# Optimization experiments

Measured on AMD Instinct MI355X. Metric: run time of the kernel, lower is better.

The kernel has to match this reference:

```python
import jax, jax.numpy as jnp
import numpy as np

N, E, F, K = 20000, 320000, 64, 256


def _lin(k, fan_in, shape):
    s = 1.0 / np.sqrt(fan_in)
    return jax.random.uniform(k, shape, jnp.float32, -s, s)


def setup_inputs() -> dict:
    key = jax.random.key(0)
    ks = jax.random.split(key, 18)
    x = jax.random.normal(ks[0], (N, F), jnp.float32)
    row = jax.random.randint(ks[1], (E,), 0, N, jnp.int32)
    off = jax.random.randint(ks[2], (E,), 1, N, jnp.int32)
    col = (row + off) % N  # no self-loops; they are added inside reference
    edge_index = jnp.stack([row, col])
    return {
        "x": x,
        "edge_index": edge_index,
        # GCN conv stack (embedding_sizes=[64,64,64] -> two convs)
        "W0": _lin(ks[3], F, (F, F)), "b0": _lin(ks[4], F, (F,)),
        "W1": _lin(ks[5], F, (F, F)), "b1": _lin(ks[6], F, (F,)),
        # ASAPooling: lin(F,F), att(2F,1)
        "lin_W": _lin(ks[7], F, (F, F)), "lin_b": _lin(ks[8], F, (F,)),
        "att_W": _lin(ks[9], 2 * F, (2 * F,)), "att_b": _lin(ks[10], 2 * F, ()),
        # LEConv(F,1): lin1 (bias), lin2 (no bias), lin3 (bias)
        "le1_W": _lin(ks[11], F, (F,)), "le1_b": _lin(ks[12], F, ()),
        "le2_W": _lin(ks[13], F, (F,)),
        "le3_W": _lin(ks[14], F, (F,)), "le3_b": _lin(ks[15], F, ()),
    }


def reference(x, edge_index, W0, b0, W1, b1, lin_W, lin_b, att_W, att_b,
              le1_W, le1_b, le2_W, le3_W, le3_b):
    n = x.shape[0]
    loop = jnp.arange(n, dtype=edge_index.dtype)
    row = jnp.concatenate([edge_index[0], loop])  # source j
    col = jnp.concatenate([edge_index[1], loop])  # target i
    w = jnp.ones(row.shape[0], x.dtype)           # edge weights (incl. self-loops)

    # --- GCNConv stack (symmetric normalization, self-loops, weight 1) ---
    deg = jax.ops.segment_sum(w, col, num_segments=n)
    dis = jax.lax.rsqrt(deg)  # deg >= 1 thanks to self-loops
    norm = dis[row] * w * dis[col]

    def gcn(h, W, b):
        h = h @ W
        return jax.ops.segment_sum(norm[:, None] * h[row], col, num_segments=n) + b

    x = jax.nn.relu(gcn(x, W0, b0))
    x = jax.nn.relu(gcn(x, W1, b1))

    # --- ASAPooling attention scoring ---
    x_pool_j = x[row]                                            # [E', F]
    x_q = jax.ops.segment_max(x_pool_j, col, num_segments=n)    # max over incoming
    x_q = x_q @ lin_W + lin_b
    score = jnp.concatenate([x_q[col], x_pool_j], axis=-1) @ att_W + att_b  # [E']
    score = jax.nn.leaky_relu(score, 0.2)
    # segment softmax over target node
    smax = jax.ops.segment_max(score, col, num_segments=n)
    e = jnp.exp(score - smax[col])
    score = e / jax.ops.segment_sum(e, col, num_segments=n)[col]

    # cluster representations
    xc = jax.ops.segment_sum(x[row] * score[:, None], col, num_segments=n)  # [N, F]

    # --- LEConv fitness: sum_j w_ij*(lin1(x_j) - lin2(x_i)) + lin3(x_i) ---
    a = xc @ le1_W + le1_b
    b = xc @ le2_W
    agg = jax.ops.segment_sum(w * (a[row] - b[col]), col, num_segments=n)
    fitness = jax.nn.sigmoid(agg + xc @ le3_W + le3_b)           # [N]

    # --- top-k selection (single graph) ---
    fit_k, perm = jax.lax.top_k(fitness, K)
    x_new = xc[perm] * fit_k[:, None]                            # [K, F]

    # --- graph coarsening: A_new = S^T A S, S = score matrix cols at perm ---
    inv = jnp.full((n,), K, jnp.int32).at[perm].set(jnp.arange(K, dtype=jnp.int32))
    Sd = jnp.zeros((n, K + 1), x.dtype).at[row, inv[col]].add(score)
    S = Sd[:, :K]                                                # [N, K]
    AS = jax.ops.segment_sum(w[:, None] * S[col], row, num_segments=n)  # A @ S
    A_new = S.T @ AS                                             # [K, K]
    A_new = A_new.at[jnp.arange(K), jnp.arange(K)].set(1.0)      # fill_diag(1)

    return (x_new, A_new, perm)
```

## Files before the change

### kernel.cpp

```cpp
#include <hip/hip_runtime.h>
#include <math.h>

constexpr int N_ = 20000;
constexpr int E_ = 320000;
constexpr int M_ = E_ + N_;
constexpr int F_ = 64;
constexpr int K_ = 256;
constexpr int TCAP = 32768;
constexpr int OUT_WORDS = K_ * F_ + K_ * K_ + K_;

constexpr size_t O_RR   = 0;
constexpr size_t O_CC   = O_RR + M_;
constexpr size_t O_CSRC = O_CC + M_;
constexpr size_t O_CNRM = O_CSRC + M_;
constexpr size_t O_SC   = O_CNRM + M_;
constexpr size_t O_BUFA = O_SC + M_;
constexpr size_t O_BUFB = O_BUFA + (size_t)N_ * F_;
constexpr size_t O_BUFC = O_BUFB + (size_t)N_ * F_;
constexpr size_t O_CPTR = O_BUFC + (size_t)N_ * F_;
constexpr size_t O_Q2   = O_CPTR + N_ + 4;
constexpr size_t O_DEN  = O_Q2 + N_;
constexpr size_t O_AV   = O_DEN + N_;
constexpr size_t O_BV   = O_AV + N_;
constexpr size_t O_C3   = O_BV + N_;
constexpr size_t O_FIT  = O_C3 + N_;
constexpr size_t O_TPTR = O_FIT + N_;
constexpr size_t O_TI   = O_TPTR + N_ + 4;
constexpr size_t O_TK   = O_TI + TCAP;
constexpr size_t O_TV   = O_TK + TCAP;
constexpr size_t O_TIDX = O_TV + TCAP;
constexpr size_t O_PERM = O_TIDX + TCAP;
constexpr size_t O_FITS = O_PERM + K_;
constexpr size_t O_WQ   = O_FITS + K_;
constexpr size_t O_ZR   = O_WQ + 72;
constexpr size_t O_CNT  = O_ZR;
constexpr size_t O_CUR  = O_CNT + N_;
constexpr size_t O_TCNT = O_CUR + N_;
constexpr size_t O_TCUR = O_TCNT + N_;
constexpr size_t O_CTRL = O_TCUR + N_;
constexpr size_t ZR_WORDS = O_CTRL + 8 - O_ZR;

__device__ __forceinline__ float4 ld4(const float* p) { return *reinterpret_cast<const float4*>(p); }
__device__ __forceinline__ void st4(float* p, float4 v) { *reinterpret_cast<float4*>(p) = v; }

__global__ void init_k(unsigned* __restrict__ zr, float* __restrict__ dout) {
  int g = blockIdx.x * blockDim.x + threadIdx.x;
  if (g < (int)ZR_WORDS) zr[g] = 0u;
  if (g < OUT_WORDS) dout[g] = 0.0f;
}

__global__ void build_edges_k(const int* __restrict__ ei, int* __restrict__ rr,
                              int* __restrict__ cc, unsigned* __restrict__ cnt,
                              const float* __restrict__ linW, const float* __restrict__ linb,
                              const float* __restrict__ attW, float* __restrict__ wq) {
  if (blockIdx.x == gridDim.x - 1) {
    int f = threadIdx.x;
    if (f < 64) {
      float s = 0.0f;
      for (int c = 0; c < 64; ++c) s += linW[f * 64 + c] * attW[c];
      wq[f] = s;
      float b = linb[f] * attW[f];
      for (int off = 32; off; off >>= 1) b += __shfl_down(b, off);
      if (f == 0) wq[64] = b;
    }
    return;
  }
  int g = blockIdx.x * blockDim.x + threadIdx.x;
  if (g >= M_) return;
  int r, c;
  if (g < E_) { r = ei[g]; c = ei[E_ + g]; } else { r = g - E_; c = r; }
  rr[g] = r; cc[g] = c;
  atomicAdd(&cnt[c], 1u);
}

__global__ void prefix_k(const unsigned* __restrict__ cnt, unsigned* __restrict__ ptr, int n) {
  __shared__ unsigned part[1024];
  int t = threadIdx.x;
  int chunk = (n + 1023) >> 10;
  int i0 = t * chunk;
  unsigned s = 0;
  for (int j = 0; j < chunk; ++j) { int i = i0 + j; if (i < n) s += cnt[i]; }
  part[t] = s; __syncthreads();
  for (int off = 1; off < 1024; off <<= 1) {
    unsigned v = (t >= off) ? part[t - off] : 0u;
    __syncthreads();
    part[t] += v;
    __syncthreads();
  }
  unsigned run = part[t] - s;
  for (int j = 0; j < chunk; ++j) {
    int i = i0 + j;
    if (i < n) { ptr[i] = run; run += cnt[i]; }
  }
  if (t == 0) ptr[n] = part[1023];
}

__global__ void scatter_csr_k(const int* __restrict__ rr, const int* __restrict__ cc,
                              const unsigned* __restrict__ cptr, unsigned* __restrict__ cur,
                              int* __restrict__ csrc, float* __restrict__ cnrm) {
  int g = blockIdx.x * blockDim.x + threadIdx.x;
  if (g >= M_) return;
  int r = rr[g], c = cc[g];
  unsigned pos = cptr[c] + atomicAdd(&cur[c], 1u);
  csrc[pos] = r;
  float dr = (float)(cptr[r + 1] - cptr[r]);
  float dc = (float)(cptr[c + 1] - cptr[c]);
  cnrm[pos] = (1.0f / sqrtf(dr)) * (1.0f / sqrtf(dc));
}

__global__ void gemm64_k(const float* __restrict__ X, const float* __restrict__ W,
                         float* __restrict__ Y) {
  __shared__ float xs[64][64];
  __shared__ float wsh[64][64];
  int t = threadIdx.x;
  int r0 = blockIdx.x * 64;
  for (int i = 0; i < 16; ++i) {
    int idx = t + i * 256;
    wsh[idx >> 6][idx & 63] = W[idx];
  }
  for (int i = 0; i < 16; ++i) {
    int idx = t + i * 256;
    int r = idx >> 6, c = idx & 63;
    xs[r][c] = (r0 + r < N_) ? X[(size_t)(r0 + r) * F_ + c] : 0.0f;
  }
  __syncthreads();
  int c = t & 63, rg = t >> 6;
  float acc[16];
#pragma unroll
  for (int m = 0; m < 16; ++m) acc[m] = 0.0f;
  for (int k = 0; k < 64; ++k) {
    float w = wsh[k][c];
#pragma unroll
    for (int m = 0; m < 16; ++m) acc[m] += xs[rg + 4 * m][k] * w;
  }
  for (int m = 0; m < 16; ++m) {
    int r = r0 + rg + 4 * m;
    if (r < N_) Y[(size_t)r * F_ + c] = acc[m];
  }
}

template<int EPI>
__global__ void agg_gcn_k(const float* __restrict__ H, const int* __restrict__ csrc,
                          const float* __restrict__ wts, const unsigned* __restrict__ cptr,
                          const float* __restrict__ bias, float* __restrict__ Y,
                          const float* __restrict__ attW, float* __restrict__ q2) {
  int wid = blockIdx.x * (blockDim.x >> 6) + (threadIdx.x >> 6);
  int lane = threadIdx.x & 63;
  if (wid >= N_) return;
  int sub = lane >> 4, fq = lane & 15;
  unsigned p0 = cptr[wid], p1 = cptr[wid + 1];
  float ax = 0.f, ay = 0.f, az = 0.f, aw = 0.f;
  for (unsigned p = p0 + sub; p < p1; p += 4) {
    int s = csrc[p];
    float w = wts[p];
    float4 h = ld4(H + (size_t)s * F_ + 4 * fq);
    ax += w * h.x; ay += w * h.y; az += w * h.z; aw += w * h.w;
  }
#pragma unroll
  for (int off = 16; off <= 32; off <<= 1) {
    ax += __shfl_xor(ax, off); ay += __shfl_xor(ay, off);
    az += __shfl_xor(az, off); aw += __shfl_xor(aw, off);
  }
  float4 b4 = ld4(bias + 4 * fq);
  ax = fmaxf(ax + b4.x, 0.f); ay = fmaxf(ay + b4.y, 0.f);
  az = fmaxf(az + b4.z, 0.f); aw = fmaxf(aw + b4.w, 0.f);
  if (sub == 0) { float4 o{ax, ay, az, aw}; st4(Y + (size_t)wid * F_ + 4 * fq, o); }
  if (EPI == 1) {
    float4 a4 = ld4(attW + 64 + 4 * fq);
    float v = ax * a4.x + ay * a4.y + az * a4.z + aw * a4.w;
#pragma unroll
    for (int off = 1; off <= 8; off <<= 1) v += __shfl_xor(v, off);
    if (lane == 0) q2[wid] = v;
  }
}

__global__ void attn_fused_k(const float* __restrict__ X2, const int* __restrict__ csrc,
                             const unsigned* __restrict__ cptr, const float* __restrict__ q2,
                             const float* __restrict__ attb, const float* __restrict__ wq,
                             float* __restrict__ sc, float* __restrict__ den,
                             float* __restrict__ XC,
                             const float* __restrict__ le1W, const float* __restrict__ le1b,
                             const float* __restrict__ le2W, const float* __restrict__ le3W,
                             const float* __restrict__ le3b, float* __restrict__ av,
                             float* __restrict__ bv, float* __restrict__ c3) {
  int wid = blockIdx.x * (blockDim.x >> 6) + (threadIdx.x >> 6);
  int lane = threadIdx.x & 63;
  if (wid >= N_) return;
  int sub = lane >> 4, fq = lane & 15;
  unsigned p0 = cptr[wid], p1 = cptr[wid + 1];
  float mx = -INFINITY, my = -INFINITY, mz = -INFINITY, mw = -INFINITY;
  for (unsigned p = p0 + sub; p < p1; p += 4) {
    int s = csrc[p];
    float4 h = ld4(X2 + (size_t)s * F_ + 4 * fq);
    mx = fmaxf(mx, h.x); my = fmaxf(my, h.y); mz = fmaxf(mz, h.z); mw = fmaxf(mw, h.w);
  }
#pragma unroll
  for (int off = 16; off <= 32; off <<= 1) {
    mx = fmaxf(mx, __shfl_xor(mx, off)); my = fmaxf(my, __shfl_xor(my, off));
    mz = fmaxf(mz, __shfl_xor(mz, off)); mw = fmaxf(mw, __shfl_xor(mw, off));
  }
  float4 w4 = ld4(wq + 4 * fq);
  float q1v = mx * w4.x + my * w4.y + mz * w4.z + mw * w4.w;
#pragma unroll
  for (int off = 1; off <= 8; off <<= 1) q1v += __shfl_xor(q1v, off);
  float base = q1v + wq[64] + attb[0];
  float m = -INFINITY;
  for (unsigned p = p0 + lane; p < p1; p += 64) {
    float s = base + q2[csrc[p]];
    s = (s > 0.0f) ? s : 0.2f * s;
    m = fmaxf(m, s);
  }
#pragma unroll
  for (int off = 1; off <= 32; off <<= 1) m = fmaxf(m, __shfl_xor(m, off));
  float d = 0.0f;
  for (unsigned p = p0 + lane; p < p1; p += 64) {
    float s = base + q2[csrc[p]];
    s = (s > 0.0f) ? s : 0.2f * s;
    float e = expf(s - m);
    sc[p] = e;
    d += e;
  }
#pragma unroll
  for (int off = 1; off <= 32; off <<= 1) d += __shfl_xor(d, off);
  if (lane == 0) den[wid] = d;
  float ax = 0.f, ay = 0.f, az = 0.f, aw = 0.f;
  for (unsigned p = p0 + sub; p < p1; p += 4) {
    int s = csrc[p];
    float sv = base + q2[s];
    sv = (sv > 0.0f) ? sv : 0.2f * sv;
    float w = expf(sv - m);
    float4 h = ld4(X2 + (size_t)s * F_ + 4 * fq);
    ax += w * h.x; ay += w * h.y; az += w * h.z; aw += w * h.w;
  }
#pragma unroll
  for (int off = 16; off <= 32; off <<= 1) {
    ax += __shfl_xor(ax, off); ay += __shfl_xor(ay, off);
    az += __shfl_xor(az, off); aw += __shfl_xor(aw, off);
  }
  float inv = 1.0f / d;
  ax *= inv; ay *= inv; az *= inv; aw *= inv;
  if (sub == 0) { float4 o{ax, ay, az, aw}; st4(XC + (size_t)wid * F_ + 4 * fq, o); }
  float4 l1 = ld4(le1W + 4 * fq), l2 = ld4(le2W + 4 * fq), l3 = ld4(le3W + 4 * fq);
  float s1 = ax * l1.x + ay * l1.y + az * l1.z + aw * l1.w;
  float s2 = ax * l2.x + ay * l2.y + az * l2.z + aw * l2.w;
  float s3 = ax * l3.x + ay * l3.y + az * l3.z + aw * l3.w;
#pragma unroll
  for (int off = 1; off <= 8; off <<= 1) {
    s1 += __shfl_xor(s1, off); s2 += __shfl_xor(s2, off); s3 += __shfl_xor(s3, off);
  }
  if (lane == 0) { av[wid] = s1 + le1b[0]; bv[wid] = s2; c3[wid] = s3 + le3b[0]; }
}

__global__ void fitness_k(const unsigned* __restrict__ cptr, const int* __restrict__ csrc,
                          const float* __restrict__ av, const float* __restrict__ bv,
                          const float* __restrict__ c3, float* __restrict__ fit) {
  int wid = blockIdx.x * (blockDim.x >> 6) + (threadIdx.x >> 6);
  int lane = threadIdx.x & 63;
  if (wid >= N_) return;
  unsigned p0 = cptr[wid], p1 = cptr[wid + 1];
  float s = 0.0f;
  for (unsigned p = p0 + lane; p < p1; p += 64) s += av[csrc[p]];
#pragma unroll
  for (int off = 1; off <= 32; off <<= 1) s += __shfl_xor(s, off);
  if (lane == 0) {
    float deg = (float)(p1 - p0);
    float val = s - deg * bv[wid] + c3[wid];
    fit[wid] = 1.0f / (1.0f + expf(-val));
  }
}

__global__ __launch_bounds__(1024) void topk_k(const float* __restrict__ fit,
                                               unsigned* __restrict__ perm_i,
                                               float* __restrict__ fit_s,
                                               float* __restrict__ out_perm) {
  __shared__ unsigned hist[256 * 16];
  __shared__ unsigned scan_[256];
  __shared__ unsigned long long keys[K_];
  __shared__ unsigned s_pfx, s_rem, s_cnt, s_bstar, s_rem2, s_cut, s_all;
  int t = threadIdx.x;
  int sub = t & 15;

  unsigned msk = 0, pfx = 0, rem = K_;
  for (int lvl = 0; lvl < 4; ++lvl) {
    int shift = 24 - lvl * 8;
    for (int i = t; i < 256 * 16; i += 1024) hist[i] = 0;
    __syncthreads();
    for (int i = t; i < N_; i += 1024) {
      unsigned fb = __float_as_uint(fit[i]);
      if ((fb & msk) == pfx)
        atomicAdd(&hist[(((fb >> shift) & 0xFF) << 4) + sub], 1u);
    }
    __syncthreads();
    unsigned h = 0;
    if (t < 256) {
      for (int s = 0; s < 16; ++s) h += hist[(t << 4) + s];
      scan_[t] = h;
    }
    __syncthreads();
    for (int off = 1; off < 256; off <<= 1) {
      unsigned v = 0;
      if (t < 256 && t + off < 256) v = scan_[t + off];
      __syncthreads();
      if (t < 256) scan_[t] += v;
      __syncthreads();
    }
    if (t < 256) {
      unsigned suf = scan_[t];
      unsigned sufn = (t < 255) ? scan_[t + 1] : 0u;
      if (suf >= rem && sufn < rem) {
        s_pfx = pfx | ((unsigned)t << shift);
        s_rem = rem - sufn;
      }
    }
    __syncthreads();
    pfx = s_pfx; rem = s_rem; msk |= (0xFFu << shift);
    __syncthreads();
  }
  if (t == 0) { s_cnt = 0; s_all = 0; }
  for (int i = t; i < 256 * 16; i += 1024) hist[i] = 0;
  __syncthreads();
  for (int i = t; i < N_; i += 1024) {
    unsigned fb = __float_as_uint(fit[i]);
    if (fb > pfx) {
      unsigned j = atomicAdd(&s_cnt, 1u);
      keys[j] = ((unsigned long long)fb << 32) | (unsigned long long)(0xFFFFFFFFu - (unsigned)i);
    } else if (fb == pfx) {
      atomicAdd(&hist[((i >> 7) << 4) + sub], 1u);
    }
  }
  __syncthreads();
  {
    unsigned h = 0;
    if (t < 256) {
      for (int s = 0; s < 16; ++s) h += hist[(t << 4) + s];
      scan_[t] = h;
    }
    __syncthreads();
    for (int off = 1; off < 256; off <<= 1) {
      unsigned v = 0;
      if (t < 256 && t >= off) v = scan_[t - off];
      __syncthreads();
      if (t < 256) scan_[t] += v;
      __syncthreads();
    }
    if (t < 256) {
      unsigned pre = scan_[t];
      unsigned prev = (t > 0) ? scan_[t - 1] : 0u;
      if (t == 255 && pre == rem) s_all = 1u;
      if (pre >= rem && prev < rem) { s_bstar = (unsigned)t; s_rem2 = rem - prev; }
    }
    __syncthreads();
  }
  unsigned bstar = s_bstar, rem2 = s_rem2;
  if (s_all) {
    for (int i = t; i < N_; i += 1024)
      if (__float_as_uint(fit[i]) == pfx) {
        unsigned j = atomicAdd(&s_cnt, 1u);
        keys[j] = ((unsigned long long)pfx << 32) | (unsigned long long)(0xFFFFFFFFu - (unsigned)i);
      }
  } else {
    for (int i = t; i < 256 * 16; i += 1024) hist[i] = 0;
    __syncthreads();
    for (int i = t; i < N_; i += 1024)
      if (__float_as_uint(fit[i]) == pfx && (unsigned)(i >> 7) == bstar)
        atomicAdd(&hist[((i & 127) << 4) + sub], 1u);
    __syncthreads();
    unsigned h = 0;
    if (t < 128) {
      for (int s = 0; s < 16; ++s) h += hist[(t << 4) + s];
      scan_[t] = h;
    }
    __syncthreads();
    for (int off = 1; off < 128; off <<= 1) {
      unsigned v = 0;
      if (t < 128 && t >= off) v = scan_[t - off];
      __syncthreads();
      if (t < 128) scan_[t] += v;
      __syncthreads();
    }
    if (t < 128) {
      unsigned pre = scan_[t];
      unsigned prev = (t > 0) ? scan_[t - 1] : 0u;
      if (pre >= rem2 && prev < rem2) s_cut = (unsigned)t;
    }
    __syncthreads();
    unsigned cut = s_cut;
    for (int i = t; i < N_; i += 1024) {
      if (__float_as_uint(fit[i]) == pfx) {
        unsigned hi = (unsigned)(i >> 7), lo = (unsigned)(i & 127);
        if (hi < bstar || (hi == bstar && lo <= cut)) {
          unsigned j = atomicAdd(&s_cnt, 1u);
          keys[j] = ((unsigned long long)pfx << 32) | (unsigned long long)(0xFFFFFFFFu - (unsigned)i);
        }
      }
    }
  }
  __syncthreads();
  for (unsigned k = 2; k <= (unsigned)K_; k <<= 1) {
    for (unsigned j = k >> 1; j > 0; j >>= 1) {
      unsigned long long nv = 0;
      if (t < K_) {
        unsigned partner = (unsigned)t ^ j;
        unsigned long long a = keys[t], b = keys[partner];
        bool desc = ((t & k) == 0);
        bool tFirst = ((unsigned)t < partner);
        unsigned long long mx2 = (a > b) ? a : b;
        unsigned long long mn = (a > b) ? b : a;
        nv = (desc == tFirst) ? mx2 : mn;
      }
      __syncthreads();
      if (t < K_) keys[t] = nv;
      __syncthreads();
    }
  }
  if (t < K_) {
    unsigned long long kk = keys[t];
    unsigned idx = 0xFFFFFFFFu - (unsigned)(kk & 0xFFFFFFFFu);
    perm_i[t] = idx;
    fit_s[t] = __uint_as_float((unsigned)(kk >> 32));
    out_perm[t] = (float)idx;
  }
}

__global__ void xnew_k(const float* __restrict__ XC, const unsigned* __restrict__ perm_i,
                       const float* __restrict__ fit_s, float* __restrict__ out) {
  int g = blockIdx.x * blockDim.x + threadIdx.x;
  if (g >= K_ * F_ / 4) return;
  int k = g >> 4, fq = g & 15;
  float4 v = ld4(XC + (size_t)perm_i[k] * F_ + 4 * fq);
  float f = fit_s[k];
  v.x *= f; v.y *= f; v.z *= f; v.w *= f;
  st4(out + (size_t)k * F_ + 4 * fq, v);
}

__global__ void trip_sel_k(const unsigned* __restrict__ perm_i, const unsigned* __restrict__ cptr,
                           const int* __restrict__ csrc, const float* __restrict__ sc,
                           const float* __restrict__ den,
                           int* __restrict__ ti, int* __restrict__ tk, float* __restrict__ tv,
                           unsigned* __restrict__ tcnt, unsigned* __restrict__ ctrl) {
  int k = blockIdx.x * blockDim.x + threadIdx.x;
  if (k >= K_) return;
  unsigned i = perm_i[k];
  unsigned p0 = cptr[i], p1 = cptr[i + 1];
  float d = den[i];
  for (unsigned p = p0; p < p1; ++p) {
    unsigned j = atomicAdd(&ctrl[5], 1u);
    if (j < (unsigned)TCAP) {
      int r = csrc[p];
      ti[j] = r; tk[j] = k; tv[j] = sc[p] / d;
      atomicAdd(&tcnt[r], 1u);
    }
  }
}

__global__ void trip_scatter_k(const int* __restrict__ ti, const unsigned* __restrict__ tptr,
                               unsigned* __restrict__ tcur, unsigned* __restrict__ tidx,
                               const unsigned* __restrict__ ctrl) {
  int g = blockIdx.x * blockDim.x + threadIdx.x;
  unsigned cnt = ctrl[5]; if (cnt > (unsigned)TCAP) cnt = TCAP;
  if (g >= (int)cnt) return;
  int i = ti[g];
  unsigned pos = tptr[i] + atomicAdd(&tcur[i], 1u);
  tidx[pos] = (unsigned)g;
}

__global__ void anew_k(const int* __restrict__ rr, const int* __restrict__ cc,
                       const unsigned* __restrict__ tptr, const unsigned* __restrict__ tidx,
                       const int* __restrict__ tk, const float* __restrict__ tv,
                       float* __restrict__ A) {
  int g = blockIdx.x * blockDim.x + threadIdx.x;
  if (g >= M_) return;
  int i = rr[g], j = cc[g];
  unsigned a0 = tptr[i], a1 = tptr[i + 1];
  if (a0 == a1) return;
  unsigned b0 = tptr[j], b1 = tptr[j + 1];
  if (b0 == b1) return;
  for (unsigned pa = a0; pa < a1; ++pa) {
    unsigned ta = tidx[pa];
    int k1 = tk[ta];
    float va = tv[ta];
    float* Arow = A + (size_t)k1 * K_;
    for (unsigned pb = b0; pb < b1; ++pb) {
      unsigned tb = tidx[pb];
      atomicAdd(&Arow[tk[tb]], va * tv[tb]);
    }
  }
}

__global__ void adiag_k(float* __restrict__ A) {
  int t = threadIdx.x;
  if (t < K_) A[(size_t)t * K_ + t] = 1.0f;
}

extern "C" void kernel_launch(void* const* d_in, const int* in_sizes, int n_in,
                              void* d_out, int out_size, void* d_ws, size_t ws_size,
                              hipStream_t stream) {
  const float* x     = (const float*)d_in[0];
  const int*   ei    = (const int*)d_in[1];
  const float* W0    = (const float*)d_in[2];
  const float* b0    = (const float*)d_in[3];
  const float* W1    = (const float*)d_in[4];
  const float* b1    = (const float*)d_in[5];
  const float* linW  = (const float*)d_in[6];
  const float* linb  = (const float*)d_in[7];
  const float* attW  = (const float*)d_in[8];
  const float* attb  = (const float*)d_in[9];
  const float* le1W  = (const float*)d_in[10];
  const float* le1b  = (const float*)d_in[11];
  const float* le2W  = (const float*)d_in[12];
  const float* le3W  = (const float*)d_in[13];
  const float* le3b  = (const float*)d_in[14];

  float*    wf = (float*)d_ws;
  unsigned* wu = (unsigned*)d_ws;
  int*      wi = (int*)d_ws;
  float*    out = (float*)d_out;

  int*      rr    = wi + O_RR;
  int*      cc    = wi + O_CC;
  int*      csrc  = wi + O_CSRC;
  float*    cnrm  = wf + O_CNRM;
  float*    sc    = wf + O_SC;
  float*    bufA  = wf + O_BUFA;
  float*    bufB  = wf + O_BUFB;
  float*    bufC  = wf + O_BUFC;
  unsigned* cptr  = wu + O_CPTR;
  float*    q2    = wf + O_Q2;
  float*    den   = wf + O_DEN;
  float*    av    = wf + O_AV;
  float*    bv    = wf + O_BV;
  float*    c3    = wf + O_C3;
  float*    fit   = wf + O_FIT;
  unsigned* tptr  = wu + O_TPTR;
  int*      ti    = wi + O_TI;
  int*      tk    = wi + O_TK;
  float*    tv    = wf + O_TV;
  unsigned* tidx  = wu + O_TIDX;
  unsigned* perm_i= wu + O_PERM;
  float*    fit_s = wf + O_FITS;
  float*    wq    = wf + O_WQ;
  unsigned* zr    = wu + O_ZR;
  unsigned* cnt   = wu + O_CNT;
  unsigned* cur   = wu + O_CUR;
  unsigned* tcnt  = wu + O_TCNT;
  unsigned* tcur  = wu + O_TCUR;
  unsigned* ctrl  = wu + O_CTRL;

  const int TB = 256;
  const int gM = (M_ + TB - 1) / TB;
  const int gW = (N_ + 3) / 4;
  const int gG = (N_ + 63) / 64;
  const int gZ = ((int)(ZR_WORDS > OUT_WORDS ? ZR_WORDS : OUT_WORDS) + TB - 1) / TB;

  hipLaunchKernelGGL(init_k, dim3(gZ), dim3(TB), 0, stream, zr, out);
  hipLaunchKernelGGL(build_edges_k, dim3(gM + 1), dim3(TB), 0, stream, ei, rr, cc, cnt,
                     linW, linb, attW, wq);
  hipLaunchKernelGGL(prefix_k, dim3(1), dim3(1024), 0, stream, cnt, cptr, N_);
  hipLaunchKernelGGL(scatter_csr_k, dim3(gM), dim3(TB), 0, stream, rr, cc, cptr, cur, csrc, cnrm);

  hipLaunchKernelGGL(gemm64_k, dim3(gG), dim3(TB), 0, stream, x, W0, bufA);
  hipLaunchKernelGGL((agg_gcn_k<0>), dim3(gW), dim3(TB), 0, stream, bufA, csrc, cnrm, cptr, b0, bufB,
                     nullptr, nullptr);
  hipLaunchKernelGGL(gemm64_k, dim3(gG), dim3(TB), 0, stream, bufB, W1, bufA);
  hipLaunchKernelGGL((agg_gcn_k<1>), dim3(gW), dim3(TB), 0, stream, bufA, csrc, cnrm, cptr, b1, bufC,
                     attW, q2);

  hipLaunchKernelGGL(attn_fused_k, dim3(gW), dim3(TB), 0, stream, bufC, csrc, cptr, q2, attb, wq,
                     sc, den, bufB, le1W, le1b, le2W, le3W, le3b, av, bv, c3);

  hipLaunchKernelGGL(fitness_k, dim3(gW), dim3(TB), 0, stream, cptr, csrc, av, bv, c3, fit);
  hipLaunchKernelGGL(topk_k, dim3(1), dim3(1024), 0, stream, fit, perm_i, fit_s, out + K_ * F_ + K_ * K_);
  hipLaunchKernelGGL(xnew_k, dim3((K_ * F_ / 4 + TB - 1) / TB), dim3(TB), 0, stream, bufB, perm_i, fit_s, out);

  hipLaunchKernelGGL(trip_sel_k, dim3(1), dim3(TB), 0, stream, perm_i, cptr, csrc, sc, den, ti, tk, tv, tcnt, ctrl);
  hipLaunchKernelGGL(prefix_k, dim3(1), dim3(1024), 0, stream, tcnt, tptr, N_);
  hipLaunchKernelGGL(trip_scatter_k, dim3(TCAP / TB), dim3(TB), 0, stream, ti, tptr, tcur, tidx, ctrl);
  hipLaunchKernelGGL(anew_k, dim3(gM), dim3(TB), 0, stream, rr, cc, tptr, tidx, tk, tv, out + K_ * F_);
  hipLaunchKernelGGL(adiag_k, dim3(1), dim3(TB), 0, stream, out + K_ * F_);

  (void)in_sizes; (void)n_in; (void)out_size; (void)ws_size;
}
```

Measured before the change: 356.6 us.

## Drop rr/cc edge copies, wave-shuffle scans, and rank-sort top-k in shared memory

Removes the materialized rr/cc edge arrays and reads edge_index directly in the scatter and A_new kernels. The prefix kernel and top-k radix select now stage data in LDS and replace the many-barrier Hillis-Steele scans with wave-level shuffle scans. The bitonic sort of the 256 selected keys is replaced by a rank-by-counting pass with atomic rank accumulation. The aim is to cut global traffic and the barrier count in the single-block kernels, at the cost of large static LDS buffers (N_ words).

Result: faster. 299.8 us (-15.9%).

```diff
diff --git a/kernel.cpp b/kernel.cpp
--- a/kernel.cpp
+++ b/kernel.cpp
@@ -9,9 +9,7 @@
 constexpr int TCAP = 32768;
 constexpr int OUT_WORDS = K_ * F_ + K_ * K_ + K_;
 
-constexpr size_t O_RR   = 0;
-constexpr size_t O_CC   = O_RR + M_;
-constexpr size_t O_CSRC = O_CC + M_;
+constexpr size_t O_CSRC = 0;
 constexpr size_t O_CNRM = O_CSRC + M_;
 constexpr size_t O_SC   = O_CNRM + M_;
 constexpr size_t O_BUFA = O_SC + M_;
@@ -49,8 +47,7 @@
   if (g < OUT_WORDS) dout[g] = 0.0f;
 }
 
-__global__ void build_edges_k(const int* __restrict__ ei, int* __restrict__ rr,
-                              int* __restrict__ cc, unsigned* __restrict__ cnt,
+__global__ void build_edges_k(const int* __restrict__ ei, unsigned* __restrict__ cnt,
                               const float* __restrict__ linW, const float* __restrict__ linb,
                               const float* __restrict__ attW, float* __restrict__ wq) {
   if (blockIdx.x == gridDim.x - 1) {
@@ -67,40 +64,53 @@
   }
   int g = blockIdx.x * blockDim.x + threadIdx.x;
   if (g >= M_) return;
-  int r, c;
-  if (g < E_) { r = ei[g]; c = ei[E_ + g]; } else { r = g - E_; c = r; }
-  rr[g] = r; cc[g] = c;
+  int c = (g < E_) ? ei[E_ + g] : g - E_;
   atomicAdd(&cnt[c], 1u);
 }
 
-__global__ void prefix_k(const unsigned* __restrict__ cnt, unsigned* __restrict__ ptr, int n) {
-  __shared__ unsigned part[1024];
+__global__ __launch_bounds__(1024) void prefix_k(const unsigned* __restrict__ cnt,
+                                                 unsigned* __restrict__ ptr, int n) {
+  __shared__ unsigned buf[N_];
+  __shared__ unsigned wsum[16];
+  __shared__ unsigned s_total;
   int t = threadIdx.x;
+  int wv = t >> 6, ln = t & 63;
+  for (int i = t; i < n; i += 1024) buf[i] = cnt[i];
+  __syncthreads();
   int chunk = (n + 1023) >> 10;
   int i0 = t * chunk;
   unsigned s = 0;
-  for (int j = 0; j < chunk; ++j) { int i = i0 + j; if (i < n) s += cnt[i]; }
-  part[t] = s; __syncthreads();
-  for (int off = 1; off < 1024; off <<= 1) {
-    unsigned v = (t >= off) ? part[t - off] : 0u;
-    __syncthreads();
-    part[t] += v;
-    __syncthreads();
-  }
-  unsigned run = part[t] - s;
+  for (int j = 0; j < chunk; ++j) { int i = i0 + j; if (i < n) s += buf[i]; }
+  unsigned pre = s;
+  for (int off = 1; off < 64; off <<= 1) {
+    unsigned v = __shfl_up(pre, off);
+    if (ln >= off) pre += v;
+  }
+  if (ln == 63) wsum[wv] = pre;
+  __syncthreads();
+  if (t == 0) {
+    unsigned run = 0;
+    for (int w = 0; w < 16; ++w) { unsigned v = wsum[w]; wsum[w] = run; run += v; }
+    s_total = run;
+  }
+  __syncthreads();
+  unsigned run = wsum[wv] + (pre - s);
   for (int j = 0; j < chunk; ++j) {
     int i = i0 + j;
-    if (i < n) { ptr[i] = run; run += cnt[i]; }
-  }
-  if (t == 0) ptr[n] = part[1023];
-}
-
-__global__ void scatter_csr_k(const int* __restrict__ rr, const int* __restrict__ cc,
+    if (i < n) { unsigned v = buf[i]; buf[i] = run; run += v; }
+  }
+  __syncthreads();
+  for (int i = t; i < n; i += 1024) ptr[i] = buf[i];
+  if (t == 0) ptr[n] = s_total;
+}
+
+__global__ void scatter_csr_k(const int* __restrict__ ei,
                               const unsigned* __restrict__ cptr, unsigned* __restrict__ cur,
                               int* __restrict__ csrc, float* __restrict__ cnrm) {
   int g = blockIdx.x * blockDim.x + threadIdx.x;
   if (g >= M_) return;
-  int r = rr[g], c = cc[g];
+  int r, c;
+  if (g < E_) { r = ei[g]; c = ei[E_ + g]; } else { r = g - E_; c = r; }
   unsigned pos = cptr[c] + atomicAdd(&cur[c], 1u);
   csrc[pos] = r;
   float dr = (float)(cptr[r + 1] - cptr[r]);
@@ -273,54 +283,64 @@
                                                unsigned* __restrict__ perm_i,
                                                float* __restrict__ fit_s,
                                                float* __restrict__ out_perm) {
+  __shared__ unsigned fb_s[N_];
   __shared__ unsigned hist[256 * 16];
-  __shared__ unsigned scan_[256];
+  __shared__ unsigned scn[256];
   __shared__ unsigned long long keys[K_];
+  __shared__ unsigned rnk[K_];
   __shared__ unsigned s_pfx, s_rem, s_cnt, s_bstar, s_rem2, s_cut, s_all;
   int t = threadIdx.x;
   int sub = t & 15;
+  int wv = t >> 6, ln = t & 63;
+
+  for (int i = t; i < N_; i += 1024) fb_s[i] = __float_as_uint(fit[i]);
+  if (t == 0) { s_cnt = 0; s_all = 0; }
+  if (t < K_) rnk[t] = 0;
+  __syncthreads();
 
   unsigned msk = 0, pfx = 0, rem = K_;
   for (int lvl = 0; lvl < 4; ++lvl) {
-    int shift = 24 - lvl * 8;
+    const int shift = 24 - lvl * 8;
     for (int i = t; i < 256 * 16; i += 1024) hist[i] = 0;
     __syncthreads();
     for (int i = t; i < N_; i += 1024) {
-      unsigned fb = __float_as_uint(fit[i]);
+      unsigned fb = fb_s[i];
       if ((fb & msk) == pfx)
         atomicAdd(&hist[(((fb >> shift) & 0xFF) << 4) + sub], 1u);
     }
     __syncthreads();
-    unsigned h = 0;
     if (t < 256) {
+      unsigned h = 0;
+#pragma unroll
       for (int s = 0; s < 16; ++s) h += hist[(t << 4) + s];
-      scan_[t] = h;
-    }
-    __syncthreads();
-    for (int off = 1; off < 256; off <<= 1) {
-      unsigned v = 0;
-      if (t < 256 && t + off < 256) v = scan_[t + off];
-      __syncthreads();
-      if (t < 256) scan_[t] += v;
-      __syncthreads();
-    }
-    if (t < 256) {
-      unsigned suf = scan_[t];
-      unsigned sufn = (t < 255) ? scan_[t + 1] : 0u;
-      if (suf >= rem && sufn < rem) {
-        s_pfx = pfx | ((unsigned)t << shift);
-        s_rem = rem - sufn;
+      scn[t] = h;
+    }
+    __syncthreads();
+    if (wv == 0) {
+      unsigned b0 = scn[4 * ln], b1 = scn[4 * ln + 1], b2 = scn[4 * ln + 2], b3 = scn[4 * ln + 3];
+      unsigned loc = b0 + b1 + b2 + b3;
+      unsigned suf = loc;
+      for (int off = 1; off < 64; off <<= 1) {
+        unsigned v = __shfl_down(suf, off);
+        if (ln + off < 64) suf += v;
       }
+      unsigned above = suf - loc;
+      unsigned s3 = above + b3;
+      unsigned s2 = s3 + b2;
+      unsigned s1 = s2 + b1;
+      unsigned s0 = s1 + b0;
+      if (s0 >= rem && s1 < rem)    { s_pfx = pfx | ((unsigned)(4 * ln)     << shift); s_rem = rem - s1; }
+      if (s1 >= rem && s2 < rem)    { s_pfx = pfx | ((unsigned)(4 * ln + 1) << shift); s_rem = rem - s2; }
+      if (s2 >= rem && s3 < rem)    { s_pfx = pfx | ((unsigned)(4 * ln + 2) << shift); s_rem = rem - s3; }
+      if (s3 >= rem && above < rem) { s_pfx = pfx | ((unsigned)(4 * ln + 3) << shift); s_rem = rem - above; }
     }
     __syncthreads();
     pfx = s_pfx; rem = s_rem; msk |= (0xFFu << shift);
-    __syncthreads();
-  }
-  if (t == 0) { s_cnt = 0; s_all = 0; }
+  }
   for (int i = t; i < 256 * 16; i += 1024) hist[i] = 0;
   __syncthreads();
   for (int i = t; i < N_; i += 1024) {
-    unsigned fb = __float_as_uint(fit[i]);
+    unsigned fb = fb_s[i];
     if (fb > pfx) {
       unsigned j = atomicAdd(&s_cnt, 1u);
       keys[j] = ((unsigned long long)fb << 32) | (unsigned long long)(0xFFFFFFFFu - (unsigned)i);
@@ -329,32 +349,37 @@
     }
   }
   __syncthreads();
-  {
+  if (t < 256) {
     unsigned h = 0;
-    if (t < 256) {
-      for (int s = 0; s < 16; ++s) h += hist[(t << 4) + s];
-      scan_[t] = h;
-    }
-    __syncthreads();
-    for (int off = 1; off < 256; off <<= 1) {
-      unsigned v = 0;
-      if (t < 256 && t >= off) v = scan_[t - off];
-      __syncthreads();
-      if (t < 256) scan_[t] += v;
-      __syncthreads();
-    }
-    if (t < 256) {
-      unsigned pre = scan_[t];
-      unsigned prev = (t > 0) ? scan_[t - 1] : 0u;
-      if (t == 255 && pre == rem) s_all = 1u;
-      if (pre >= rem && prev < rem) { s_bstar = (unsigned)t; s_rem2 = rem - prev; }
-    }
-    __syncthreads();
-  }
+#pragma unroll
+    for (int s = 0; s < 16; ++s) h += hist[(t << 4) + s];
+    scn[t] = h;
+  }
+  __syncthreads();
+  if (wv == 0) {
+    unsigned b0 = scn[4 * ln], b1 = scn[4 * ln + 1], b2 = scn[4 * ln + 2], b3 = scn[4 * ln + 3];
+    unsigned loc = b0 + b1 + b2 + b3;
+    unsigned pre = loc;
+    for (int off = 1; off < 64; off <<= 1) {
+      unsigned v = __shfl_up(pre, off);
+      if (ln >= off) pre += v;
+    }
+    unsigned below = pre - loc;
+    unsigned p0 = below + b0;
+    unsigned p1 = p0 + b1;
+    unsigned p2 = p1 + b2;
+    unsigned p3 = p2 + b3;
+    if (ln == 63 && p3 == rem) s_all = 1u;
+    if (p0 >= rem && below < rem) { s_bstar = 4u * ln;     s_rem2 = rem - below; }
+    if (p1 >= rem && p0 < rem)    { s_bstar = 4u * ln + 1; s_rem2 = rem - p0; }
+    if (p2 >= rem && p1 < rem)    { s_bstar = 4u * ln + 2; s_rem2 = rem - p1; }
+    if (p3 >= rem && p2 < rem)    { s_bstar = 4u * ln + 3; s_rem2 = rem - p2; }
+  }
+  __syncthreads();
   unsigned bstar = s_bstar, rem2 = s_rem2;
   if (s_all) {
     for (int i = t; i < N_; i += 1024)
-      if (__float_as_uint(fit[i]) == pfx) {
+      if (fb_s[i] == pfx) {
         unsigned j = atomicAdd(&s_cnt, 1u);
         keys[j] = ((unsigned long long)pfx << 32) | (unsigned long long)(0xFFFFFFFFu - (unsigned)i);
       }
@@ -362,31 +387,34 @@
     for (int i = t; i < 256 * 16; i += 1024) hist[i] = 0;
     __syncthreads();
     for (int i = t; i < N_; i += 1024)
-      if (__float_as_uint(fit[i]) == pfx && (unsigned)(i >> 7) == bstar)
+      if (fb_s[i] == pfx && (unsigned)(i >> 7) == bstar)
         atomicAdd(&hist[((i & 127) << 4) + sub], 1u);
     __syncthreads();
-    unsigned h = 0;
     if (t < 128) {
+      unsigned h = 0;
+#pragma unroll
       for (int s = 0; s < 16; ++s) h += hist[(t << 4) + s];
-      scan_[t] = h;
-    }
-    __syncthreads();
-    for (int off = 1; off < 128; off <<= 1) {
-      unsigned v = 0;
-      if (t < 128 && t >= off) v = scan_[t - off];
-      __syncthreads();
-      if (t < 128) scan_[t] += v;
-      __syncthreads();
-    }
-    if (t < 128) {
-      unsigned pre = scan_[t];
-      unsigned prev = (t > 0) ? scan_[t - 1] : 0u;
-      if (pre >= rem2 && prev < rem2) s_cut = (unsigned)t;
+      scn[t] = h;
+    }
+    __syncthreads();
+    if (wv == 0) {
+      unsigned b0 = scn[2 * ln], b1 = scn[2 * ln + 1];
+      unsigned loc = b0 + b1;
+      unsigned pre = loc;
+      for (int off = 1; off < 64; off <<= 1) {
+        unsigned v = __shfl_up(pre, off);
+        if (ln >= off) pre += v;
+      }
+      unsigned below = pre - loc;
+      unsigned p0 = below + b0;
+      unsigned p1 = p0 + b1;
+      if (p0 >= rem2 && below < rem2) s_cut = 2u * ln;
+      if (p1 >= rem2 && p0 < rem2)    s_cut = 2u * ln + 1;
     }
     __syncthreads();
     unsigned cut = s_cut;
     for (int i = t; i < N_; i += 1024) {
-      if (__float_as_uint(fit[i]) == pfx) {
+      if (fb_s[i] == pfx) {
         unsigned hi = (unsigned)(i >> 7), lo = (unsigned)(i & 127);
         if (hi < bstar || (hi == bstar && lo <= cut)) {
           unsigned j = atomicAdd(&s_cnt, 1u);
@@ -396,29 +424,21 @@
     }
   }
   __syncthreads();
-  for (unsigned k = 2; k <= (unsigned)K_; k <<= 1) {
-    for (unsigned j = k >> 1; j > 0; j >>= 1) {
-      unsigned long long nv = 0;
-      if (t < K_) {
-        unsigned partner = (unsigned)t ^ j;
-        unsigned long long a = keys[t], b = keys[partner];
-        bool desc = ((t & k) == 0);
-        bool tFirst = ((unsigned)t < partner);
-        unsigned long long mx2 = (a > b) ? a : b;
-        unsigned long long mn = (a > b) ? b : a;
-        nv = (desc == tFirst) ? mx2 : mn;
-      }
-      __syncthreads();
-      if (t < K_) keys[t] = nv;
-      __syncthreads();
-    }
-  }
+  {
+    int k = t & 255, seg = t >> 8;
+    unsigned long long my = keys[k];
+    unsigned r = 0;
+    for (int j = seg * 64; j < seg * 64 + 64; ++j) r += (keys[j] > my) ? 1u : 0u;
+    if (r) atomicAdd(&rnk[k], r);
+  }
+  __syncthreads();
   if (t < K_) {
     unsigned long long kk = keys[t];
+    unsigned r = rnk[t];
     unsigned idx = 0xFFFFFFFFu - (unsigned)(kk & 0xFFFFFFFFu);
-    perm_i[t] = idx;
-    fit_s[t] = __uint_as_float((unsigned)(kk >> 32));
-    out_perm[t] = (float)idx;
+    perm_i[r] = idx;
+    fit_s[r] = __uint_as_float((unsigned)(kk >> 32));
+    out_perm[r] = (float)idx;
   }
 }
 
@@ -464,13 +484,14 @@
   tidx[pos] = (unsigned)g;
 }
 
-__global__ void anew_k(const int* __restrict__ rr, const int* __restrict__ cc,
+__global__ void anew_k(const int* __restrict__ ei,
                        const unsigned* __restrict__ tptr, const unsigned* __restrict__ tidx,
                        const int* __restrict__ tk, const float* __restrict__ tv,
                        float* __restrict__ A) {
   int g = blockIdx.x * blockDim.x + threadIdx.x;
   if (g >= M_) return;
-  int i = rr[g], j = cc[g];
+  int i, j;
+  if (g < E_) { i = ei[g]; j = ei[E_ + g]; } else { i = j = g - E_; }
   unsigned a0 = tptr[i], a1 = tptr[i + 1];
   if (a0 == a1) return;
   unsigned b0 = tptr[j], b1 = tptr[j + 1];
@@ -516,8 +537,6 @@
   int*      wi = (int*)d_ws;
   float*    out = (float*)d_out;
 
-  int*      rr    = wi + O_RR;
-  int*      cc    = wi + O_CC;
   int*      csrc  = wi + O_CSRC;
   float*    cnrm  = wf + O_CNRM;
   float*    sc    = wf + O_SC;
@@ -553,10 +572,10 @@
   const int gZ = ((int)(ZR_WORDS > OUT_WORDS ? ZR_WORDS : OUT_WORDS) + TB - 1) / TB;
 
   hipLaunchKernelGGL(init_k, dim3(gZ), dim3(TB), 0, stream, zr, out);
-  hipLaunchKernelGGL(build_edges_k, dim3(gM + 1), dim3(TB), 0, stream, ei, rr, cc, cnt,
+  hipLaunchKernelGGL(build_edges_k, dim3(gM + 1), dim3(TB), 0, stream, ei, cnt,
                      linW, linb, attW, wq);
   hipLaunchKernelGGL(prefix_k, dim3(1), dim3(1024), 0, stream, cnt, cptr, N_);
-  hipLaunchKernelGGL(scatter_csr_k, dim3(gM), dim3(TB), 0, stream, rr, cc, cptr, cur, csrc, cnrm);
+  hipLaunchKernelGGL(scatter_csr_k, dim3(gM), dim3(TB), 0, stream, ei, cptr, cur, csrc, cnrm);
 
   hipLaunchKernelGGL(gemm64_k, dim3(gG), dim3(TB), 0, stream, x, W0, bufA);
   hipLaunchKernelGGL((agg_gcn_k<0>), dim3(gW), dim3(TB), 0, stream, bufA, csrc, cnrm, cptr, b0, bufB,
@@ -575,7 +594,7 @@
   hipLaunchKernelGGL(trip_sel_k, dim3(1), dim3(TB), 0, stream, perm_i, cptr, csrc, sc, den, ti, tk, tv, tcnt, ctrl);
   hipLaunchKernelGGL(prefix_k, dim3(1), dim3(1024), 0, stream, tcnt, tptr, N_);
   hipLaunchKernelGGL(trip_scatter_k, dim3(TCAP / TB), dim3(TB), 0, stream, ti, tptr, tcur, tidx, ctrl);
-  hipLaunchKernelGGL(anew_k, dim3(gM), dim3(TB), 0, stream, rr, cc, tptr, tidx, tk, tv, out + K_ * F_);
+  hipLaunchKernelGGL(anew_k, dim3(gM), dim3(TB), 0, stream, ei, tptr, tidx, tk, tv, out + K_ * F_);
   hipLaunchKernelGGL(adiag_k, dim3(1), dim3(TB), 0, stream, out + K_ * F_);
 
   (void)in_sizes; (void)n_in; (void)out_size; (void)ws_size;
```
